# Kernel tuning notes

Hardware: AMD Instinct MI355X
Metric: run time of the kernel (lower is better)

Reference implementation:

```python
import jax, jax.numpy as jnp
import numpy as np
import math

G = 512        # graphs in batch
N_PER = 256    # nodes per graph (regular batching)
H = 128        # hidden_size == rnn_hidden_size
DEG = 8        # avg degree
RATIO = 0.8    # TopKPooling ratio
N = G * N_PER
E = N * DEG
N_HIDDEN = 3   # n_hidden_layers


def setup_inputs() -> dict:
    key = jax.random.key(0)
    ks = jax.random.split(key, 20)
    x = jax.random.normal(ks[0], (N, H), jnp.float32)
    m = N_PER * DEG
    src_l = jax.random.randint(ks[1], (G, m), 0, N_PER)
    dst_l = jax.random.randint(ks[2], (G, m), 0, N_PER)
    off = (jnp.arange(G, dtype=jnp.int32) * N_PER)[:, None]
    edge_index = jnp.stack([(src_l + off).reshape(-1), (dst_l + off).reshape(-1)]).astype(jnp.int32)
    s = 1.0 / math.sqrt(H)
    def w(k, shape):
        return jax.random.normal(k, shape, jnp.float32) * s
    return {
        'x': x, 'edge_index': edge_index,
        'W0': w(ks[3], (H, H)), 'b0': jnp.zeros((H,), jnp.float32), 'p0': w(ks[4], (H,)),
        'W1': w(ks[5], (H, H)), 'b1': jnp.zeros((H,), jnp.float32), 'p1': w(ks[6], (H,)),
        'W2': w(ks[7], (H, H)), 'b2': jnp.zeros((H,), jnp.float32), 'p2': w(ks[8], (H,)),
        'Wg': w(ks[9], (H, 1)), 'bg': jnp.zeros((1,), jnp.float32),
    }


def _gcn(x, src, dst, w_e, W, b, n_nodes):
    # GCNConv with self loops: out = D^-1/2 (A+I) D^-1/2 (x W) + b, masked edges have w_e=0
    h = x @ W
    deg = jax.ops.segment_sum(w_e, dst, num_segments=n_nodes) + 1.0  # +1 self loop
    dinv = jax.lax.rsqrt(deg)
    norm = w_e * dinv[src] * dinv[dst]
    agg = jax.ops.segment_sum(h[src] * norm[:, None], dst, num_segments=n_nodes)
    agg = agg + h * (dinv * dinv)[:, None]   # self-loop term
    return agg + b


def _topk(x, src, dst, w_e, p, n_per):
    # TopKPooling: score = x.p/||p||, keep top ceil(ratio*n) per graph, scale by tanh(score)
    k = math.ceil(RATIO * n_per)
    score = (x @ p) / jnp.linalg.norm(p)
    _, idx = jax.lax.top_k(score.reshape(G, n_per), k)           # [G,k] local idx
    perm = (idx + (jnp.arange(G, dtype=idx.dtype) * n_per)[:, None]).reshape(-1)
    x_new = x[perm] * jnp.tanh(score[perm])[:, None]
    nmap = jnp.full((G * n_per,), -1, jnp.int32).at[perm].set(jnp.arange(G * k, dtype=jnp.int32))
    ms, md = nmap[src], nmap[dst]
    valid = (ms >= 0) & (md >= 0)
    src2 = jnp.where(valid, ms, 0)
    dst2 = jnp.where(valid, md, 0)
    return x_new, src2, dst2, w_e * valid.astype(w_e.dtype), k


def _attpool(x, n_per, Wg, bg):
    # GlobalAttention: softmax(gate) over nodes of each graph, weighted sum
    gate = (x @ Wg + bg).reshape(G, n_per)
    a = jax.nn.softmax(gate, axis=1)
    return jnp.einsum('gn,gnh->gh', a, x.reshape(G, n_per, H))


def reference(x, edge_index, W0, b0, p0, W1, b1, p1, W2, b2, p2, Wg, bg):
    src, dst = edge_index[0], edge_index[1]
    w_e = jnp.ones((E,), jnp.float32)
    n_per = N_PER
    h = jax.nn.relu(_gcn(x, src, dst, w_e, W0, b0, G * n_per))
    h, src, dst, w_e, n_per = _topk(h, src, dst, w_e, p0, n_per)
    out = _attpool(h, n_per, Wg, bg)
    for (W, b, p) in ((W1, b1, p1), (W2, b2, p2)):  # n_hidden_layers - 1 = 2
        h = jax.nn.relu(_gcn(h, src, dst, w_e, W, b, G * n_per))
        h, src, dst, w_e, n_per = _topk(h, src, dst, w_e, p, n_per)
        out = out + _attpool(h, n_per, Wg, bg)
    return out
```

## Files before the change

kernel.cpp:

```cpp
#include <hip/hip_runtime.h>
#include <math.h>

#define GCOUNT 512
#define HDIM 128
#define EPG 2048
#define E_TOTAL (GCOUNT * EPG)
#define DEADE 0xFFFFFFFFu

typedef __attribute__((ext_vector_type(8))) short short8;
typedef __attribute__((ext_vector_type(4))) float f32x4;

__device__ inline unsigned short f2bf(float f) {
  unsigned int u = __float_as_uint(f);
  return (unsigned short)((u + 0x7FFFu + ((u >> 16) & 1u)) >> 16);
}
__device__ inline float bf2f(unsigned short s) {
  return __uint_as_float(((unsigned int)s) << 16);
}
__device__ inline float4 z4() { return make_float4(0.f, 0.f, 0.f, 0.f); }
__device__ inline float4 ld4(const float* p) { return *(const float4*)p; }
__device__ inline void fma4(float4& u, float w, float4 x) {
  u.x = fmaf(w, x.x, u.x); u.y = fmaf(w, x.y, u.y);
  u.z = fmaf(w, x.z, u.z); u.w = fmaf(w, x.w, u.w);
}
__device__ inline float4 fin4(float4 u, float4 s, float4 b, float dv) {
  float4 r;
  r.x = fmaxf(fmaf(dv, fmaf(s.x, dv, u.x), b.x), 0.f);
  r.y = fmaxf(fmaf(dv, fmaf(s.y, dv, u.y), b.y), 0.f);
  r.z = fmaxf(fmaf(dv, fmaf(s.z, dv, u.z), b.z), 0.f);
  r.w = fmaxf(fmaf(dv, fmaf(s.w, dv, u.w), b.w), 0.f);
  return r;
}
__device__ inline float dot4(float4 a, float4 b) {
  return a.x * b.x + a.y * b.y + a.z * b.z + a.w * b.w;
}
__device__ inline float4 scale4(float4 v, float s) {
  v.x *= s; v.y *= s; v.z *= s; v.w *= s; return v;
}

__global__ __launch_bounds__(256) void k_wsplit(const float* __restrict__ W,
                                                unsigned short* __restrict__ out) {
  int t = blockIdx.x * 256 + threadIdx.x;
  int lane = t & 63;
  int ct = (t >> 6) & 7;
  int kc = t >> 9;
  int kbase = kc * 32 + (lane >> 4) * 8;
  int col = ct * 16 + (lane & 15);
#pragma unroll
  for (int j = 0; j < 8; j++) {
    float w = W[(size_t)(kbase + j) * HDIM + col];
    unsigned short h0 = f2bf(w);  float g0 = bf2f(h0);
    unsigned short h1 = f2bf(w - g0);
    int base = (kc * 8 + ct) * 512 + lane * 8 + j;
    out[base]         = h0;
    out[base + 16384] = h1;
  }
}

__global__ __launch_bounds__(1024, 1) void k_net(
    const float* __restrict__ xIn, const int* __restrict__ ei0,
    const unsigned short* __restrict__ Ws0,
    const unsigned short* __restrict__ Ws1,
    const unsigned short* __restrict__ Ws2,
    const float* __restrict__ b0, const float* __restrict__ p0,
    const float* __restrict__ b1, const float* __restrict__ p1,
    const float* __restrict__ b2, const float* __restrict__ p2,
    const float* __restrict__ Wg, const float* __restrict__ bgp,
    float* __restrict__ outp) {

  __shared__ __align__(16) float h_s[256 * 132];
  __shared__ unsigned int es[EPG];
  __shared__ unsigned short ss[EPG];
  __shared__ __align__(16) int deg[256];
  __shared__ int cnt[256];
  __shared__ int ofs[256];
  __shared__ int rp[260];
  __shared__ float dinv_s[256];
  __shared__ float rawsc_s[256];
  __shared__ float hd[256];
  __shared__ float sc[256];
  __shared__ int   idx[256];
  __shared__ float tn[256];
  __shared__ float accout[128];
  __shared__ float part[512];
  __shared__ float red[8];
  __shared__ float snorm_s;

  int g = blockIdx.x, t = threadIdx.x;
  int lane = t & 63, wv = t >> 6;
  int eb = g * EPG;
  float bgv = bgp[0];

  if (t < 256) deg[t] = 0;
  if (t < 128) accout[t] = 0.f;
  __syncthreads();
  {
    const float4* xg = (const float4*)(xIn + (size_t)g * 256 * HDIM);
    for (int i = t; i < 8192; i += 1024) {
      int r = i >> 5, q = i & 31;
      *(float4*)&h_s[r * 132 + (q << 2)] = xg[i];
    }
  }
#pragma unroll
  for (int q = 0; q < 2; q++) {
    int e = t + q * 1024;
    int s_ = ei0[eb + e] - g * 256;
    int d_ = ei0[E_TOTAL + eb + e] - g * 256;
    es[e] = (unsigned)s_ | ((unsigned)d_ << 16);
    atomicAdd(&deg[d_], 1);
  }
  __syncthreads();

  int n = 256;
#pragma unroll 1
  for (int layer = 0; layer < 3; layer++) {
    const unsigned short* Ws = (layer == 0) ? Ws0 : (layer == 1 ? Ws1 : Ws2);
    const float* bias = (layer == 0) ? b0 : (layer == 1 ? b1 : b2);
    const float* p    = (layer == 0) ? p0 : (layer == 1 ? p1 : p2);
    int k = (layer == 0) ? 205 : (layer == 1 ? 164 : 132);
    int T = (n + 15) >> 4;

    if (wv < T) {
      int rbase = wv * 16;
      int arow = lane & 15, kgrp = (lane >> 4) * 8;
      f32x4 acc[8];
#pragma unroll
      for (int ct = 0; ct < 8; ct++) acc[ct] = (f32x4){0.f, 0.f, 0.f, 0.f};
#pragma unroll
      for (int kc = 0; kc < 4; kc++) {
        short8 fa0, fa1;
        {
          const float* ap = &h_s[(rbase + arow) * 132 + kc * 32 + kgrp];
          float4 x0 = ld4(ap);
          float4 x1 = ld4(ap + 4);
          float v[8] = {x0.x, x0.y, x0.z, x0.w, x1.x, x1.y, x1.z, x1.w};
#pragma unroll
          for (int j = 0; j < 8; j++) {
            float a = v[j];
            unsigned short q0 = f2bf(a);
            unsigned short q1 = f2bf(a - bf2f(q0));
            fa0[j] = (short)q0; fa1[j] = (short)q1;
          }
        }
#pragma unroll
        for (int ct = 0; ct < 8; ct++) {
          const unsigned short* wb = Ws + (kc * 8 + ct) * 512 + lane * 8;
          short8 w0 = *(const short8*)wb;
          short8 w1 = *(const short8*)(wb + 16384);
          acc[ct] = __builtin_amdgcn_mfma_f32_16x16x32_bf16(fa0, w0, acc[ct], 0, 0, 0);
          acc[ct] = __builtin_amdgcn_mfma_f32_16x16x32_bf16(fa0, w1, acc[ct], 0, 0, 0);
          acc[ct] = __builtin_amdgcn_mfma_f32_16x16x32_bf16(fa1, w0, acc[ct], 0, 0, 0);
          acc[ct] = __builtin_amdgcn_mfma_f32_16x16x32_bf16(fa1, w1, acc[ct], 0, 0, 0);
        }
      }
      int crow = (lane >> 4) * 4, ccol = lane & 15;
#pragma unroll
      for (int ct = 0; ct < 8; ct++)
#pragma unroll
        for (int reg = 0; reg < 4; reg++)
          h_s[(rbase + crow + reg) * 132 + ct * 16 + ccol] = acc[ct][reg];
    }
    __syncthreads();

    if (t < 256) dinv_s[t] = rsqrtf((float)deg[t] + 1.0f);
    if (wv == 0) {
      int4 c4 = *(const int4*)&deg[lane << 2];
      int s4 = c4.x + c4.y + c4.z + c4.w;
      int run = s4;
#pragma unroll
      for (int o = 1; o < 64; o <<= 1) {
        int v = __shfl_up(run, o);
        if (lane >= o) run += v;
      }
      int base = run - s4;
      int v1 = base + c4.x, v2 = v1 + c4.y, v3 = v2 + c4.z;
      int li = lane << 2;
      rp[li] = base; rp[li + 1] = v1; rp[li + 2] = v2; rp[li + 3] = v3;
      ofs[li] = base; ofs[li + 1] = v1; ofs[li + 2] = v2; ofs[li + 3] = v3;
      if (lane == 63) rp[256] = run;
    }
    if (wv == 1) {
      float q = p[lane] * p[lane] + p[lane + 64] * p[lane + 64];
#pragma unroll
      for (int o = 32; o > 0; o >>= 1) q += __shfl_xor(q, o);
      if (lane == 0) snorm_s = sqrtf(q);
    }
    if (t >= 128 && t < 512) {
      int i = t - 128;
      part[i] = (i < 128) ? bias[i] : (i < 256 ? p[i - 128] : Wg[i - 256]);
    }
    __syncthreads();

    if (t < 256) { cnt[t] = -1; deg[t] = 0; }
    for (int e = t; e < EPG; e += 1024) {
      unsigned u = es[e];
      if (u != DEADE) {
        int pos = atomicAdd(&ofs[u >> 16], 1);
        ss[pos] = (unsigned short)(u & 0xFFFFu);
      }
    }
    __syncthreads();

    {
      int dstT = t >> 2;
      int cq = (t & 3) << 3;
      bool dok = dstT < n;
      int begT = 0, endT = 0; float dvT = 0.f;
      if (dok) { begT = rp[dstT]; endT = rp[dstT + 1]; dvT = dinv_s[dstT]; }
      float sp = 0.f, sg = 0.f;
      float4 rA0, rA1, rB0, rB1;
      if (dok) {
        float4 uA0 = z4(), uA1 = z4(), uB0 = z4(), uB1 = z4();
        for (int j = begT; j < endT; ++j) {
          int sa = ss[j];
          float wa = dinv_s[sa];
          const float* ha = &h_s[sa * 132 + cq];
          fma4(uA0, wa, ld4(ha));      fma4(uA1, wa, ld4(ha + 4));
          fma4(uB0, wa, ld4(ha + 32)); fma4(uB1, wa, ld4(ha + 36));
        }
        const float* hdp = &h_s[dstT * 132 + cq];
        rA0 = fin4(uA0, ld4(hdp),      ld4(&part[cq]),      dvT);
        rA1 = fin4(uA1, ld4(hdp + 4),  ld4(&part[cq + 4]),  dvT);
        rB0 = fin4(uB0, ld4(hdp + 32), ld4(&part[32 + cq]), dvT);
        rB1 = fin4(uB1, ld4(hdp + 36), ld4(&part[32 + cq + 4]), dvT);
        sp += dot4(rA0, ld4(&part[128 + cq])) + dot4(rA1, ld4(&part[128 + cq + 4]))
            + dot4(rB0, ld4(&part[160 + cq])) + dot4(rB1, ld4(&part[160 + cq + 4]));
        sg += dot4(rA0, ld4(&part[256 + cq])) + dot4(rA1, ld4(&part[256 + cq + 4]))
            + dot4(rB0, ld4(&part[288 + cq])) + dot4(rB1, ld4(&part[288 + cq + 4]));
      }
      __syncthreads();
      if (dok) {
        float* hw = &h_s[dstT * 132 + cq];
        *(float4*)hw = rA0; *(float4*)(hw + 4) = rA1;
        *(float4*)(hw + 32) = rB0; *(float4*)(hw + 36) = rB1;
      }
      if (dok) {
        float4 uA0 = z4(), uA1 = z4(), uB0 = z4(), uB1 = z4();
        for (int j = begT; j < endT; ++j) {
          int sa = ss[j];
          float wa = dinv_s[sa];
          const float* ha = &h_s[sa * 132 + 64 + cq];
          fma4(uA0, wa, ld4(ha));      fma4(uA1, wa, ld4(ha + 4));
          fma4(uB0, wa, ld4(ha + 32)); fma4(uB1, wa, ld4(ha + 36));
        }
        const float* hdp = &h_s[dstT * 132 + 64 + cq];
        rA0 = fin4(uA0, ld4(hdp),      ld4(&part[64 + cq]),  dvT);
        rA1 = fin4(uA1, ld4(hdp + 4),  ld4(&part[64 + cq + 4]), dvT);
        rB0 = fin4(uB0, ld4(hdp + 32), ld4(&part[96 + cq]),  dvT);
        rB1 = fin4(uB1, ld4(hdp + 36), ld4(&part[96 + cq + 4]), dvT);
        sp += dot4(rA0, ld4(&part[192 + cq])) + dot4(rA1, ld4(&part[192 + cq + 4]))
            + dot4(rB0, ld4(&part[224 + cq])) + dot4(rB1, ld4(&part[224 + cq + 4]));
        sg += dot4(rA0, ld4(&part[320 + cq])) + dot4(rA1, ld4(&part[320 + cq + 4]))
            + dot4(rB0, ld4(&part[352 + cq])) + dot4(rB1, ld4(&part[352 + cq + 4]));
      }
      __syncthreads();
      if (dok) {
        float* hw = &h_s[dstT * 132 + 64 + cq];
        *(float4*)hw = rA0; *(float4*)(hw + 4) = rA1;
        *(float4*)(hw + 32) = rB0; *(float4*)(hw + 36) = rB1;
      }
      sp += __shfl_xor(sp, 1); sp += __shfl_xor(sp, 2);
      sg += __shfl_xor(sg, 1); sg += __shfl_xor(sg, 2);
      if (dok && (t & 3) == 0) { rawsc_s[dstT] = sp; hd[dstT] = sg; }
    }
    __syncthreads();

    float key = -INFINITY;
    int id = t & 255;
    if (t < n) key = rawsc_s[t];
    {
      int pp = 0;
      for (int size = 2; size <= 256; size <<= 1) {
        for (int stride = size >> 1; stride > 0; stride >>= 1) {
          if (stride > 32) {
            float* sb = pp ? (float*)part : sc;
            int* ib = pp ? ofs : idx;
            if (t < 256) { sb[t] = key; ib[t] = id; }
            __syncthreads();
            if (t < 256) {
              float pk = sb[t ^ stride];
              int pi = ib[t ^ stride];
              bool want = ((t & size) == 0);
              bool lowr = ((t & stride) == 0);
              bool mineFirst = (key > pk) || (key == pk && id < pi);
              if (mineFirst != (want == lowr)) { key = pk; id = pi; }
            }
            pp ^= 1;
          } else {
            if (t < 256) {
              float pk = __shfl_xor(key, stride);
              int pi = __shfl_xor(id, stride);
              bool want = ((t & size) == 0);
              bool lowr = ((t & stride) == 0);
              bool mineFirst = (key > pk) || (key == pk && id < pi);
              if (mineFirst != (want == lowr)) { key = pk; id = pi; }
            }
          }
        }
      }
    }
    __syncthreads();
    if (t < 256) idx[t] = id;
    __syncthreads();

    float gate = -INFINITY;
    if (t < k) {
      float tnv = tanhf(key / snorm_s);
      tn[t] = tnv;
      cnt[id] = t;
      gate = fmaf(hd[id], tnv, bgv);
    }
    if (wv < 4) {
      float m = gate;
#pragma unroll
      for (int o = 32; o > 0; o >>= 1) m = fmaxf(m, __shfl_xor(m, o));
      if (lane == 0) red[wv] = m;
    }
    __syncthreads();

    float ex = 0.f;
    if (wv < 4) {
      float m = fmaxf(fmaxf(red[0], red[1]), fmaxf(red[2], red[3]));
      ex = (t < k) ? __expf(gate - m) : 0.f;
      float s = ex;
#pragma unroll
      for (int o = 32; o > 0; o >>= 1) s += __shfl_xor(s, o);
      if (lane == 0) red[4 + wv] = s;
    } else if (wv >= 8 && layer < 2) {
      int tt = t - 512;
#pragma unroll
      for (int q = 0; q < 4; q++) {
        int e = tt + q * 512;
        unsigned u = es[e];
        unsigned o = DEADE;
        if (u != DEADE) {
          int ns = cnt[u & 0xFFFFu], nd = cnt[u >> 16];
          if (ns >= 0 && nd >= 0) o = (unsigned)ns | ((unsigned)nd << 16);
        }
        es[e] = o;
        if (o != DEADE) atomicAdd(&deg[o >> 16], 1);
      }
    }
    __syncthreads();

    if (t < 256) {
      float inv = 1.f / (red[4] + red[5] + red[6] + red[7]);
      float a = (t < k) ? ex * inv : 0.f;
      sc[t] = (layer == 2) ? a * tn[t] : a;
    }
    __syncthreads();

    if (layer < 2) {
      {
        int rT = t >> 2;
        int cq4 = (t & 3) << 3;
        bool rok = rT < k;
        int src = 0; float tr = 0.f;
        if (rok) { src = idx[rT]; tr = tn[rT]; }
        float4 vA0, vA1, vB0, vB1;
        if (rok) {
          const float* hp = &h_s[src * 132 + cq4];
          vA0 = scale4(ld4(hp), tr);      vA1 = scale4(ld4(hp + 4), tr);
          vB0 = scale4(ld4(hp + 32), tr); vB1 = scale4(ld4(hp + 36), tr);
        }
        __syncthreads();
        if (rok) {
          float* hw = &h_s[rT * 132 + cq4];
          *(float4*)hw = vA0; *(float4*)(hw + 4) = vA1;
          *(float4*)(hw + 32) = vB0; *(float4*)(hw + 36) = vB1;
        }
        if (rok) {
          const float* hp = &h_s[src * 132 + 64 + cq4];
          vA0 = scale4(ld4(hp), tr);      vA1 = scale4(ld4(hp + 4), tr);
          vB0 = scale4(ld4(hp + 32), tr); vB1 = scale4(ld4(hp + 36), tr);
        }
        __syncthreads();
        if (rok) {
          float* hw = &h_s[rT * 132 + 64 + cq4];
          *(float4*)hw = vA0; *(float4*)(hw + 4) = vA1;
          *(float4*)(hw + 32) = vB0; *(float4*)(hw + 36) = vB1;
        }
      }
      __syncthreads();
      if (t < 512) {
        int grp = t >> 7, c2 = t & 127;
        float pp2 = 0.f;
        for (int r = grp; r < k; r += 4) pp2 = fmaf(sc[r], h_s[r * 132 + c2], pp2);
        part[t] = pp2;
      }
      __syncthreads();
      if (t < 128) accout[t] += part[t] + part[128 + t] + part[256 + t] + part[384 + t];
      __syncthreads();
    } else {
      if (t < 512) {
        int grp = t >> 7, c2 = t & 127;
        float pp2 = 0.f;
        for (int r = grp; r < k; r += 4) pp2 = fmaf(sc[r], h_s[idx[r] * 132 + c2], pp2);
        part[t] = pp2;
      }
      __syncthreads();
      if (t < 128)
        outp[(size_t)g * HDIM + t] =
            accout[t] + part[t] + part[128 + t] + part[256 + t] + part[384 + t];
    }
    n = k;
  }
}

extern "C" void kernel_launch(void* const* d_in, const int* in_sizes, int n_in,
                              void* d_out, int out_size, void* d_ws, size_t ws_size,
                              hipStream_t stream) {
  const float* x  = (const float*)d_in[0];
  const int*   ei = (const int*)d_in[1];
  const float* W0 = (const float*)d_in[2];
  const float* b0 = (const float*)d_in[3];
  const float* p0 = (const float*)d_in[4];
  const float* W1 = (const float*)d_in[5];
  const float* b1 = (const float*)d_in[6];
  const float* p1 = (const float*)d_in[7];
  const float* W2 = (const float*)d_in[8];
  const float* b2 = (const float*)d_in[9];
  const float* p2 = (const float*)d_in[10];
  const float* Wg = (const float*)d_in[11];
  const float* bg = (const float*)d_in[12];
  float* out = (float*)d_out;

  unsigned char* ws = (unsigned char*)d_ws;
  unsigned short* Wsp0 = (unsigned short*)(ws);
  unsigned short* Wsp1 = (unsigned short*)(ws + 98304ull);
  unsigned short* Wsp2 = (unsigned short*)(ws + 196608ull);

  k_wsplit<<<8, 256, 0, stream>>>(W0, Wsp0);
  k_wsplit<<<8, 256, 0, stream>>>(W1, Wsp1);
  k_wsplit<<<8, 256, 0, stream>>>(W2, Wsp2);
  k_net<<<GCOUNT, 1024, 0, stream>>>(x, ei, Wsp0, Wsp1, Wsp2,
                                     b0, p0, b1, p1, b2, p2, Wg, bg, out);
}
```

Baseline: 201.3 us.

## Merge weight-split launches, prefetch edge sources, and halve sync in row compaction

Folds the three bf16 hi/lo weight-split kernels into a single 24-block launch, selecting the weight matrix per block, to save two launch overheads. Software-pipelines the GCN aggregation loops so the next source index and its dinv are loaded before the current FMAs run, hiding LDS latency. Also merges the two-pass top-k row gather into one pass that holds eight float4 registers, cutting one barrier but raising register pressure in a 1024-thread block.

```diff
diff --git a/kernel.cpp b/kernel.cpp
--- a/kernel.cpp
+++ b/kernel.cpp
@@ -38,9 +38,14 @@
   v.x *= s; v.y *= s; v.z *= s; v.w *= s; return v;
 }
 
-__global__ __launch_bounds__(256) void k_wsplit(const float* __restrict__ W,
-                                                unsigned short* __restrict__ out) {
-  int t = blockIdx.x * 256 + threadIdx.x;
+__global__ __launch_bounds__(256) void k_wsplit3(const float* __restrict__ W0,
+                                                 const float* __restrict__ W1,
+                                                 const float* __restrict__ W2,
+                                                 unsigned short* __restrict__ outAll) {
+  int b = blockIdx.x >> 3;
+  const float* W = (b == 0) ? W0 : (b == 1 ? W1 : W2);
+  unsigned short* out = outAll + b * 49152;
+  int t = (blockIdx.x & 7) * 256 + threadIdx.x;
   int lane = t & 63;
   int ct = (t >> 6) & 7;
   int kc = t >> 9;
@@ -211,12 +216,17 @@
       float4 rA0, rA1, rB0, rB1;
       if (dok) {
         float4 uA0 = z4(), uA1 = z4(), uB0 = z4(), uB1 = z4();
-        for (int j = begT; j < endT; ++j) {
-          int sa = ss[j];
-          float wa = dinv_s[sa];
+        int j = begT;
+        int sa = (j < endT) ? ss[j] : 0;
+        float wa = (j < endT) ? dinv_s[sa] : 0.f;
+        for (; j < endT; ) {
+          int jn = j + 1;
+          int sa2 = (jn < endT) ? ss[jn] : 0;
+          float wa2 = (jn < endT) ? dinv_s[sa2] : 0.f;
           const float* ha = &h_s[sa * 132 + cq];
           fma4(uA0, wa, ld4(ha));      fma4(uA1, wa, ld4(ha + 4));
           fma4(uB0, wa, ld4(ha + 32)); fma4(uB1, wa, ld4(ha + 36));
+          sa = sa2; wa = wa2; j = jn;
         }
         const float* hdp = &h_s[dstT * 132 + cq];
         rA0 = fin4(uA0, ld4(hdp),      ld4(&part[cq]),      dvT);
@@ -236,12 +246,17 @@
       }
       if (dok) {
         float4 uA0 = z4(), uA1 = z4(), uB0 = z4(), uB1 = z4();
-        for (int j = begT; j < endT; ++j) {
-          int sa = ss[j];
-          float wa = dinv_s[sa];
+        int j = begT;
+        int sa = (j < endT) ? ss[j] : 0;
+        float wa = (j < endT) ? dinv_s[sa] : 0.f;
+        for (; j < endT; ) {
+          int jn = j + 1;
+          int sa2 = (jn < endT) ? ss[jn] : 0;
+          float wa2 = (jn < endT) ? dinv_s[sa2] : 0.f;
           const float* ha = &h_s[sa * 132 + 64 + cq];
           fma4(uA0, wa, ld4(ha));      fma4(uA1, wa, ld4(ha + 4));
           fma4(uB0, wa, ld4(ha + 32)); fma4(uB1, wa, ld4(ha + 36));
+          sa = sa2; wa = wa2; j = jn;
         }
         const float* hdp = &h_s[dstT * 132 + 64 + cq];
         rA0 = fin4(uA0, ld4(hdp),      ld4(&part[64 + cq]),  dvT);
@@ -357,28 +372,21 @@
         bool rok = rT < k;
         int src = 0; float tr = 0.f;
         if (rok) { src = idx[rT]; tr = tn[rT]; }
-        float4 vA0, vA1, vB0, vB1;
+        float4 vA0, vA1, vB0, vB1, vC0, vC1, vD0, vD1;
         if (rok) {
           const float* hp = &h_s[src * 132 + cq4];
-          vA0 = scale4(ld4(hp), tr);      vA1 = scale4(ld4(hp + 4), tr);
-          vB0 = scale4(ld4(hp + 32), tr); vB1 = scale4(ld4(hp + 36), tr);
+          vA0 = scale4(ld4(hp), tr);       vA1 = scale4(ld4(hp + 4), tr);
+          vB0 = scale4(ld4(hp + 32), tr);  vB1 = scale4(ld4(hp + 36), tr);
+          vC0 = scale4(ld4(hp + 64), tr);  vC1 = scale4(ld4(hp + 68), tr);
+          vD0 = scale4(ld4(hp + 96), tr);  vD1 = scale4(ld4(hp + 100), tr);
         }
         __syncthreads();
         if (rok) {
           float* hw = &h_s[rT * 132 + cq4];
-          *(float4*)hw = vA0; *(float4*)(hw + 4) = vA1;
+          *(float4*)hw = vA0;        *(float4*)(hw + 4) = vA1;
           *(float4*)(hw + 32) = vB0; *(float4*)(hw + 36) = vB1;
-        }
-        if (rok) {
-          const float* hp = &h_s[src * 132 + 64 + cq4];
-          vA0 = scale4(ld4(hp), tr);      vA1 = scale4(ld4(hp + 4), tr);
-          vB0 = scale4(ld4(hp + 32), tr); vB1 = scale4(ld4(hp + 36), tr);
-        }
-        __syncthreads();
-        if (rok) {
-          float* hw = &h_s[rT * 132 + 64 + cq4];
-          *(float4*)hw = vA0; *(float4*)(hw + 4) = vA1;
-          *(float4*)(hw + 32) = vB0; *(float4*)(hw + 36) = vB1;
+          *(float4*)(hw + 64) = vC0; *(float4*)(hw + 68) = vC1;
+          *(float4*)(hw + 96) = vD0; *(float4*)(hw + 100) = vD1;
         }
       }
       __syncthreads();
@@ -426,13 +434,12 @@
   float* out = (float*)d_out;
 
   unsigned char* ws = (unsigned char*)d_ws;
-  unsigned short* Wsp0 = (unsigned short*)(ws);
+  unsigned short* WspA = (unsigned short*)(ws);
+  unsigned short* Wsp0 = WspA;
   unsigned short* Wsp1 = (unsigned short*)(ws + 98304ull);
   unsigned short* Wsp2 = (unsigned short*)(ws + 196608ull);
 
-  k_wsplit<<<8, 256, 0, stream>>>(W0, Wsp0);
-  k_wsplit<<<8, 256, 0, stream>>>(W1, Wsp1);
-  k_wsplit<<<8, 256, 0, stream>>>(W2, Wsp2);
+  k_wsplit3<<<24, 256, 0, stream>>>(W0, W1, W2, WspA);
   k_net<<<GCOUNT, 1024, 0, stream>>>(x, ei, Wsp0, Wsp1, Wsp2,
                                      b0, p0, b1, p1, b2, p2, Wg, bg, out);
 }
```

Result: slower. 206.3 us (+2.5%).
